# Kernel tuning notes

Hardware: AMD Instinct MI355X
Metric: run time of the kernel (lower is better)

The kernel has to match this reference:

```python
import jax, jax.numpy as jnp
import numpy as np

B = 8
A = 1614
TOPN = 6
IOU_THR = 0.25
PAD = 224
OUT = 224

def _make_anchors():
    # 6 anchor shapes on the 14x14 map, 6 on 7x7, 9 on 4x4 -> 1614 total,
    # ordered anchor-type-major then row-major spatial to match the [C,H,W] flatten
    # of the tidy conv outputs (as generate_default_anchor_maps does in NTS-Net).
    specs = [
        (14, 32.0, [(48, 48), (64, 48), (48, 64), (80, 80), (96, 64), (64, 96)]),
        (7, 64.0, [(96, 96), (128, 96), (96, 128), (160, 160), (192, 128), (128, 192)]),
        (4, 112.0, [(192, 192), (256, 192), (192, 256), (288, 288), (320, 256), (256, 320), (352, 352), (384, 320), (320, 384)]),
    ]
    blocks = []
    for fm, stride, sizes in specs:
        c = (np.arange(fm) + 0.5) * stride
        cy, cx = np.meshgrid(c, c, indexing='ij')
        for (h, w) in sizes:
            blocks.append(np.stack([cy - h / 2, cx - w / 2, cy + h / 2, cx + w / 2], -1).reshape(-1, 4))
    a = (np.concatenate(blocks, 0) + PAD).astype(np.int64)  # mimic (edge_anchors+224).astype(int)
    return a.astype(np.float32)  # [1614,4] (y0,x0,y1,x1) in padded-image coords

def _conv(x, w, b, stride, pad):
    y = jax.lax.conv_general_dilated(x, w, (stride, stride), [(pad, pad), (pad, pad)],
                                     dimension_numbers=('NCHW', 'OIHW', 'NCHW'))
    return y + b[None, :, None, None]

def _rpn_scores(rpn, wd1, bd1, wd2, bd2, wd3, bd3, wt1, bt1, wt2, bt2, wt3, bt3):
    b = rpn.shape[0]
    d1 = jax.nn.relu(_conv(rpn, wd1, bd1, 1, 1))   # [B,128,14,14]
    d2 = jax.nn.relu(_conv(d1, wd2, bd2, 2, 1))    # [B,128,7,7]
    d3 = jax.nn.relu(_conv(d2, wd3, bd3, 2, 1))    # [B,128,4,4]
    t1 = _conv(d1, wt1, bt1, 1, 0).reshape(b, -1)  # [B,1176]
    t2 = _conv(d2, wt2, bt2, 1, 0).reshape(b, -1)  # [B,294]
    t3 = _conv(d3, wt3, bt3, 1, 0).reshape(b, -1)  # [B,144]
    return jnp.concatenate([t1, t2, t3], axis=1)   # [B,1614]

def _nms_keep(boxes, scores):
    # Greedy NMS over all A anchors; returns keep mask in ORIGINAL anchor order.
    order = jnp.argsort(-scores)
    b = boxes[order]
    y0, x0, y1, x1 = b[:, 0], b[:, 1], b[:, 2], b[:, 3]
    area = (y1 - y0) * (x1 - x0)
    ih = jnp.clip(jnp.minimum(y1[:, None], y1[None, :]) - jnp.maximum(y0[:, None], y0[None, :]), 0)
    iw = jnp.clip(jnp.minimum(x1[:, None], x1[None, :]) - jnp.maximum(x0[:, None], x0[None, :]), 0)
    inter = ih * iw
    iou = inter / (area[:, None] + area[None, :] - inter)
    idx = jnp.arange(A)
    def body(i, supp):
        row = (iou[i] > IOU_THR) & (idx > i)
        return jnp.where(supp[i], supp, supp | row)
    supp = jax.lax.fori_loop(0, A, body, jnp.zeros((A,), bool))
    return jnp.zeros((A,), bool).at[order].set(~supp)

def _crop_resize(img, box):
    # img [3,Hp,Wp]; box int32 (x0,y0,x1,y1).
    # Equivalent to F.interpolate(img[:, y0:y1, x0:x1], (224,224), 'bilinear', align_corners=True)
    x0, y0, x1, y1 = box[0], box[1], box[2], box[3]
    t = jnp.arange(OUT, dtype=jnp.float32) / (OUT - 1)
    sy = y0.astype(jnp.float32) + t * (y1 - 1 - y0).astype(jnp.float32)
    sx = x0.astype(jnp.float32) + t * (x1 - 1 - x0).astype(jnp.float32)
    y0i = jnp.floor(sy).astype(jnp.int32); x0i = jnp.floor(sx).astype(jnp.int32)
    y1i = jnp.minimum(y0i + 1, y1 - 1);    x1i = jnp.minimum(x0i + 1, x1 - 1)
    wy = (sy - y0i.astype(jnp.float32))[None, :, None]
    wx = (sx - x0i.astype(jnp.float32))[None, None, :]
    g = lambda yi, xi: img[:, yi][:, :, xi]  # gather rows then cols -> [3,224,224]
    top = (1 - wx) * g(y0i, x0i) + wx * g(y0i, x1i)
    bot = (1 - wx) * g(y1i, x0i) + wx * g(y1i, x1i)
    return (1 - wy) * top + wy * bot

def setup_inputs():
    key = jax.random.key(0)
    ks = jax.random.split(key, 16)
    n = jax.random.normal
    return {
        'x': n(ks[0], (B, 3, 448, 448), jnp.float32),
        'rpn_feature': n(ks[1], (B, 2048, 14, 14), jnp.float32),
        'anchors': jnp.asarray(_make_anchors()),
        'wd1': 0.02 * n(ks[2], (128, 2048, 3, 3), jnp.float32), 'bd1': 0.01 * n(ks[3], (128,), jnp.float32),
        'wd2': 0.05 * n(ks[4], (128, 128, 3, 3), jnp.float32),  'bd2': 0.01 * n(ks[5], (128,), jnp.float32),
        'wd3': 0.05 * n(ks[6], (128, 128, 3, 3), jnp.float32),  'bd3': 0.01 * n(ks[7], (128,), jnp.float32),
        'wt1': 0.1 * n(ks[8], (6, 128, 1, 1), jnp.float32),     'bt1': 0.01 * n(ks[9], (6,), jnp.float32),
        'wt2': 0.1 * n(ks[10], (6, 128, 1, 1), jnp.float32),    'bt2': 0.01 * n(ks[11], (6,), jnp.float32),
        'wt3': 0.1 * n(ks[12], (9, 128, 1, 1), jnp.float32),    'bt3': 0.01 * n(ks[13], (9,), jnp.float32),
    }

def reference(x, rpn_feature, anchors, wd1, bd1, wd2, bd2, wd3, bd3, wt1, bt1, wt2, bt2, wt3, bt3):
    scores = _rpn_scores(rpn_feature, wd1, bd1, wd2, bd2, wd3, bd3, wt1, bt1, wt2, bt2, wt3, bt3)
    keep = jax.vmap(lambda s: _nms_keep(anchors, s))(scores)           # [B,A] bool
    masked = jnp.where(keep, scores, -jnp.inf)
    top_prob, top_idx = jax.lax.top_k(masked, TOPN)                    # [B,6]
    tb = anchors[top_idx]                                              # [B,6,4] (y0,x0,y1,x1)
    coords = jnp.stack([tb[..., 1], tb[..., 0], tb[..., 3], tb[..., 2]], -1)  # (x0,y0,x1,y1)
    x_pad = jnp.pad(x, ((0, 0), (0, 0), (PAD, PAD), (PAD, PAD)))       # [B,3,896,896]
    bint = coords.astype(jnp.int32)
    part_imgs = jax.vmap(lambda img, bs: jax.vmap(lambda bb: _crop_resize(img, bb))(bs))(x_pad, bint)  # [B,6,3,224,224]
    return part_imgs, coords, top_prob, top_idx
```

## Files before the change

### kernel.cpp

```cpp
#include <hip/hip_runtime.h>
#include <hip/hip_bf16.h>
#include <math.h>
#include <stdint.h>


#define OFF_COORDS 7225344
#define OFF_PROB   7225536
#define OFF_IDX    7225584
#define NA 1614
#define K1TOT 18432

typedef __attribute__((ext_vector_type(8)))  short  short8;
typedef __attribute__((ext_vector_type(16))) float  floatx16;

__global__ __launch_bounds__(256) void k_prep_a(const float* __restrict__ rpn,
                                                __hip_bfloat16* __restrict__ ah,
                                                __hip_bfloat16* __restrict__ al)
{
    __shared__ float tile[64][65];
    const int cib  = blockIdx.x * 64;
    const int posb = blockIdx.y * 64;
    const int b    = blockIdx.z;
    const int t    = threadIdx.x;
#pragma unroll
    for (int it = 0; it < 16; ++it) {
        int idx  = it * 256 + t;
        int cil  = idx >> 6;
        int posl = idx & 63;
        int pos  = posb + posl;
        int py = pos >> 4, px = pos & 15;
        int y = py - 1, x = px - 1;
        float v = 0.0f;
        if ((unsigned)y < 14u && (unsigned)x < 14u)
            v = rpn[((size_t)(b * 2048 + cib + cil) * 14 + y) * 14 + x];
        tile[cil][posl] = v;
    }
    __syncthreads();
#pragma unroll
    for (int it = 0; it < 16; ++it) {
        int idx  = it * 256 + t;
        int posl = idx >> 6;
        int cil  = idx & 63;
        float v = tile[cil][posl];
        __hip_bfloat16 h = __float2bfloat16(v);
        __hip_bfloat16 l = __float2bfloat16(v - __bfloat162float(h));
        size_t o = (size_t)(b * 256 + posb + posl) * 2048 + cib + cil;
        ah[o] = h; al[o] = l;
    }
}

__global__ __launch_bounds__(256) void k_prep_b(const float* __restrict__ w,
                                                __hip_bfloat16* __restrict__ bh,
                                                __hip_bfloat16* __restrict__ bl)
{
    const int tap = blockIdx.x;
    const int co  = blockIdx.y;
    const int t   = threadIdx.x;
#pragma unroll
    for (int i = 0; i < 8; ++i) {
        int ci = i * 256 + t;
        float v = w[((size_t)co * 2048 + ci) * 9 + tap];
        __hip_bfloat16 h = __float2bfloat16(v);
        __hip_bfloat16 l = __float2bfloat16(v - __bfloat162float(h));
        size_t o = (size_t)co * K1TOT + tap * 2048 + ci;
        bh[o] = h; bl[o] = l;
    }
}

__global__ __launch_bounds__(128) void k_prep_w23(const float* __restrict__ w2,
                                                  const float* __restrict__ w3,
                                                  __hip_bfloat16* __restrict__ b2h,
                                                  __hip_bfloat16* __restrict__ b2l,
                                                  __hip_bfloat16* __restrict__ b3h,
                                                  __hip_bfloat16* __restrict__ b3l)
{
    const int tap = blockIdx.x;
    const int co  = blockIdx.y;
    const int z   = blockIdx.z;
    const int ci  = threadIdx.x;
    const float* w = z ? w3 : w2;
    __hip_bfloat16* bh = z ? b3h : b2h;
    __hip_bfloat16* bl = z ? b3l : b2l;
    float v = w[((size_t)co * 128 + ci) * 9 + tap];
    __hip_bfloat16 h = __float2bfloat16(v);
    __hip_bfloat16 l = __float2bfloat16(v - __bfloat162float(h));
    size_t o = (size_t)co * 1152 + tap * 128 + ci;
    bh[o] = h; bl[o] = l;
}

template<int POSN, int OW, int STR, int CIN, int MTOT>
__global__ __launch_bounds__(256) void k_conv_mfma(const short* __restrict__ ah,
                                                   const short* __restrict__ al,
                                                   const short* __restrict__ bh,
                                                   const short* __restrict__ bl,
                                                   float* __restrict__ partial,
                                                   int chunk)
{
    constexpr int KTOT = CIN * 9;
    __shared__ short AsH[128][40];
    __shared__ short AsL[128][40];
    __shared__ short BsH[128][40];
    __shared__ short BsL[128][40];

    const int t     = threadIdx.x;
    const int lane  = t & 63;
    const int w     = t >> 6;
    const int wm    = (w & 1) * 64;
    const int wn    = (w >> 1) * 64;
    const int lm    = lane & 31;
    const int half  = lane >> 5;
    const int mbase = blockIdx.x * 128;
    const int k0    = blockIdx.y * chunk;
    const int k1    = (k0 + chunk < KTOT) ? (k0 + chunk) : KTOT;

    int arow[2], apos[2]; bool aval[2];
    const int akc = (t & 3) * 8;
#pragma unroll
    for (int i = 0; i < 2; ++i) {
        int row = ((i * 256 + t) >> 2);
        int m   = mbase + row;
        arow[i] = row;
        aval[i] = (m < MTOT);
        int mm = aval[i] ? m : 0;
        int b  = mm / POSN;
        int p  = mm - b * POSN;
        int y  = p / OW;
        int x  = p - y * OW;
        apos[i] = b * 256 + y * STR * 16 + x * STR;
    }

    floatx16 acc[2][2];
#pragma unroll
    for (int mf = 0; mf < 2; ++mf)
#pragma unroll
        for (int nf = 0; nf < 2; ++nf)
#pragma unroll
            for (int r = 0; r < 16; ++r) acc[mf][nf][r] = 0.0f;

    const short8 zero8 = {0, 0, 0, 0, 0, 0, 0, 0};

    for (int ks = k0; ks < k1; ks += 32) {
        const int tap = ks / CIN;
        const int ci0 = ks - tap * CIN;
        const int dy  = tap / 3, dx = tap - dy * 3;
#pragma unroll
        for (int i = 0; i < 2; ++i) {
            short8 vh = zero8, vl = zero8;
            if (aval[i]) {
                size_t g = (size_t)(apos[i] + dy * 16 + dx) * CIN + ci0 + akc;
                vh = *(const short8*)(ah + g);
                vl = *(const short8*)(al + g);
            }
            *(short8*)&AsH[arow[i]][akc] = vh;
            *(short8*)&AsL[arow[i]][akc] = vl;
        }
#pragma unroll
        for (int i = 0; i < 2; ++i) {
            int n = ((i * 256 + t) >> 2);
            size_t g = (size_t)n * KTOT + ks + akc;
            *(short8*)&BsH[n][akc] = *(const short8*)(bh + g);
            *(short8*)&BsL[n][akc] = *(const short8*)(bl + g);
        }
        __syncthreads();
#pragma unroll
        for (int kst = 0; kst < 2; ++kst) {
            const int koff = kst * 16 + half * 8;
            short8 a_h[2], a_l[2], b_h[2], b_l[2];
#pragma unroll
            for (int mf = 0; mf < 2; ++mf) {
                a_h[mf] = *(const short8*)&AsH[wm + mf * 32 + lm][koff];
                a_l[mf] = *(const short8*)&AsL[wm + mf * 32 + lm][koff];
            }
#pragma unroll
            for (int nf = 0; nf < 2; ++nf) {
                b_h[nf] = *(const short8*)&BsH[wn + nf * 32 + lm][koff];
                b_l[nf] = *(const short8*)&BsL[wn + nf * 32 + lm][koff];
            }
#pragma unroll
            for (int mf = 0; mf < 2; ++mf)
#pragma unroll
                for (int nf = 0; nf < 2; ++nf) {
                    acc[mf][nf] = __builtin_amdgcn_mfma_f32_32x32x16_bf16(
                        a_h[mf], b_h[nf], acc[mf][nf], 0, 0, 0);
                    acc[mf][nf] = __builtin_amdgcn_mfma_f32_32x32x16_bf16(
                        a_h[mf], b_l[nf], acc[mf][nf], 0, 0, 0);
                    acc[mf][nf] = __builtin_amdgcn_mfma_f32_32x32x16_bf16(
                        a_l[mf], b_h[nf], acc[mf][nf], 0, 0, 0);
                }
        }
        __syncthreads();
    }

    float* P = partial + (size_t)blockIdx.y * MTOT * 128;
#pragma unroll
    for (int mf = 0; mf < 2; ++mf)
#pragma unroll
        for (int nf = 0; nf < 2; ++nf)
#pragma unroll
            for (int r = 0; r < 16; ++r) {
                int row = (r & 3) + 8 * (r >> 2) + 4 * half;
                int m = mbase + wm + mf * 32 + row;
                int n = wn + nf * 32 + lm;
                if (m < MTOT) P[(size_t)m * 128 + n] = acc[mf][nf][r];
            }
}

template<int POSN, int OWV>
__global__ __launch_bounds__(256) void k_reduce_pad(const float* __restrict__ partial,
                                                    const float* __restrict__ bias,
                                                    float* __restrict__ dn,
                                                    __hip_bfloat16* __restrict__ ph,
                                                    __hip_bfloat16* __restrict__ pl,
                                                    int S)
{
    constexpr int MTOT = 8 * POSN;
    int idx = blockIdx.x * 256 + threadIdx.x;
    int b   = idx >> 15;
    int pos = (idx >> 7) & 255;
    int co  = idx & 127;
    int y = (pos >> 4) - 1;
    int x = (pos & 15) - 1;
    if ((unsigned)y < (unsigned)OWV && (unsigned)x < (unsigned)OWV) {
        int m = b * POSN + y * OWV + x;
        float s = bias[co];
        for (int k = 0; k < S; ++k) s += partial[(size_t)k * MTOT * 128 + m * 128 + co];
        s = fmaxf(s, 0.0f);
        dn[(size_t)m * 128 + co] = s;
        __hip_bfloat16 h = __float2bfloat16(s);
        __hip_bfloat16 l = __float2bfloat16(s - __bfloat162float(h));
        ph[idx] = h; pl[idx] = l;
    } else {
        ph[idx] = __float2bfloat16(0.0f);
        pl[idx] = __float2bfloat16(0.0f);
    }
}

__global__ __launch_bounds__(256) void k_reduce3(const float* __restrict__ partial,
                                                 const float* __restrict__ bias,
                                                 float* __restrict__ dn, int S)
{
    int idx = blockIdx.x * 256 + threadIdx.x;
    int co  = idx & 127;
    float s = bias[co];
    for (int k = 0; k < S; ++k) s += partial[(size_t)k * 128 * 128 + idx];
    dn[idx] = fmaxf(s, 0.0f);
}

__global__ __launch_bounds__(256) void k_heads(const float* __restrict__ d1n,
                                               const float* __restrict__ d2n,
                                               const float* __restrict__ d3n,
                                               const float* __restrict__ w1, const float* __restrict__ b1,
                                               const float* __restrict__ w2, const float* __restrict__ b2,
                                               const float* __restrict__ w3, const float* __restrict__ b3,
                                               float* __restrict__ scores)
{
    int idx = blockIdx.x * 256 + threadIdx.x;
    if (idx >= 8 * NA) return;
    int b = idx / NA;
    int e = idx - b * NA;
    const float* d; const float* w; float bias;
    if (e < 1176) {
        int c = e / 196, p = e - c * 196;
        d = d1n + (size_t)(b * 196 + p) * 128; w = w1 + c * 128; bias = b1[c];
    } else if (e < 1470) {
        int e2 = e - 1176; int c = e2 / 49, p = e2 - c * 49;
        d = d2n + (size_t)(b * 49 + p) * 128; w = w2 + c * 128; bias = b2[c];
    } else {
        int e2 = e - 1470; int c = e2 / 16, p = e2 - c * 16;
        d = d3n + (size_t)(b * 16 + p) * 128; w = w3 + c * 128; bias = b3[c];
    }
    float s = bias;
#pragma unroll
    for (int i = 0; i < 32; ++i) {
        float4 dv = ((const float4*)d)[i];
        float4 wv = ((const float4*)w)[i];
        s = fmaf(dv.x, wv.x, s);
        s = fmaf(dv.y, wv.y, s);
        s = fmaf(dv.z, wv.z, s);
        s = fmaf(dv.w, wv.w, s);
    }
    scores[idx] = s;
}

__global__ __launch_bounds__(256) void k_nms_topk(const float* __restrict__ scores,
                                                  const float* __restrict__ anchors,
                                                  float* __restrict__ out,
                                                  int* __restrict__ boxes)
{
    __shared__ float ms[NA];
    __shared__ float ay0[NA], ax0[NA], ay1[NA], ax1[NA];
    __shared__ unsigned char picked[NA];
    __shared__ float rv[4]; __shared__ int ri[4];
    __shared__ float win[5];
    int b = blockIdx.x;
    int t = threadIdx.x;
    for (int i = t; i < NA; i += 256) {
        ms[i] = scores[b * NA + i];
        float4 an = ((const float4*)anchors)[i];
        ay0[i] = an.x; ax0[i] = an.y; ay1[i] = an.z; ax1[i] = an.w;
        picked[i] = 0;
    }
    __syncthreads();
    for (int r = 0; r < 6; ++r) {
        float bv = -INFINITY; int bi = NA;
        for (int i = t; i < NA; i += 256) {
            if (!picked[i]) {
                float v = ms[i];
                if (v > bv || (v == bv && i < bi)) { bv = v; bi = i; }
            }
        }
#pragma unroll
        for (int off = 32; off > 0; off >>= 1) {
            float v2 = __shfl_down(bv, off);
            int   i2 = __shfl_down(bi, off);
            if (v2 > bv || (v2 == bv && i2 < bi)) { bv = v2; bi = i2; }
        }
        if ((t & 63) == 0) { rv[t >> 6] = bv; ri[t >> 6] = bi; }
        __syncthreads();
        if (t == 0) {
            bv = rv[0]; bi = ri[0];
            for (int wv = 1; wv < 4; ++wv)
                if (rv[wv] > bv || (rv[wv] == bv && ri[wv] < bi)) { bv = rv[wv]; bi = ri[wv]; }
            picked[bi] = 1;
            win[0] = ay0[bi]; win[1] = ax0[bi]; win[2] = ay1[bi]; win[3] = ax1[bi]; win[4] = bv;
            int o = b * 6 + r;
            out[OFF_COORDS + o * 4 + 0] = ax0[bi];
            out[OFF_COORDS + o * 4 + 1] = ay0[bi];
            out[OFF_COORDS + o * 4 + 2] = ax1[bi];
            out[OFF_COORDS + o * 4 + 3] = ay1[bi];
            out[OFF_PROB + o] = bv;
            out[OFF_IDX  + o] = (float)bi;
            boxes[o * 4 + 0] = (int)ax0[bi];
            boxes[o * 4 + 1] = (int)ay0[bi];
            boxes[o * 4 + 2] = (int)ax1[bi];
            boxes[o * 4 + 3] = (int)ay1[bi];
        }
        __syncthreads();
        float by0 = win[0], bx0 = win[1], by1 = win[2], bx1 = win[3];
        float barea = (by1 - by0) * (bx1 - bx0);
        for (int i = t; i < NA; i += 256) {
            if (picked[i]) continue;
            float ih = fmaxf(fminf(by1, ay1[i]) - fmaxf(by0, ay0[i]), 0.0f);
            float iw = fmaxf(fminf(bx1, ax1[i]) - fmaxf(bx0, ax0[i]), 0.0f);
            float inter = ih * iw;
            float area  = (ay1[i] - ay0[i]) * (ax1[i] - ax0[i]);
            float iou = inter / (barea + area - inter);
            if (iou > 0.25f) ms[i] = -INFINITY;
        }
        __syncthreads();
    }
}

__global__ __launch_bounds__(256) void k_crop(const float* __restrict__ x,
                                              const int* __restrict__ boxes,
                                              float* __restrict__ out)
{
    int bid = blockIdx.x;
    int i = threadIdx.x;
    if (i >= 224) return;
    int j   = bid % 224;
    int rem = bid / 224;
    int c   = rem % 3;
    int br  = rem / 3;
    int b   = br / 6;
    int4 bx = ((const int4*)boxes)[br];
    float tj = (float)j / 223.0f;
    float sy = (float)bx.y + tj * (float)(bx.w - 1 - bx.y);
    int y0i = (int)floorf(sy);
    int y1i = min(y0i + 1, bx.w - 1);
    float wy = sy - (float)y0i;
    float ti = (float)i / 223.0f;
    float sx = (float)bx.x + ti * (float)(bx.z - 1 - bx.x);
    int x0i = (int)floorf(sx);
    int x1i = min(x0i + 1, bx.z - 1);
    float wx = sx - (float)x0i;
    const float* img = x + ((size_t)b * 3 + c) * 448 * 448;
    auto g = [&](int yy, int xx) -> float {
        yy -= 224; xx -= 224;
        if ((unsigned)yy >= 448u || (unsigned)xx >= 448u) return 0.0f;
        return img[(size_t)yy * 448 + xx];
    };
    float g00 = g(y0i, x0i), g01 = g(y0i, x1i);
    float g10 = g(y1i, x0i), g11 = g(y1i, x1i);
    float top = (1.0f - wx) * g00 + wx * g01;
    float bot = (1.0f - wx) * g10 + wx * g11;
    out[(size_t)bid * 224 + i] = (1.0f - wy) * top + wy * bot;
}

extern "C" void kernel_launch(void* const* d_in, const int* in_sizes, int n_in,
                              void* d_out, int out_size, void* d_ws, size_t ws_size,
                              hipStream_t stream)
{
    (void)in_sizes; (void)n_in; (void)out_size;
    const float* x    = (const float*)d_in[0];
    const float* rpn  = (const float*)d_in[1];
    const float* anch = (const float*)d_in[2];
    const float* wd1  = (const float*)d_in[3];
    const float* bd1  = (const float*)d_in[4];
    const float* wd2  = (const float*)d_in[5];
    const float* bd2  = (const float*)d_in[6];
    const float* wd3  = (const float*)d_in[7];
    const float* bd3  = (const float*)d_in[8];
    const float* hw1  = (const float*)d_in[9];
    const float* hb1  = (const float*)d_in[10];
    const float* hw2  = (const float*)d_in[11];
    const float* hb2  = (const float*)d_in[12];
    const float* hw3  = (const float*)d_in[13];
    const float* hb3  = (const float*)d_in[14];
    float* out = (float*)d_out;

    char* ws = (char*)d_ws;
    size_t off = 0;
    auto alloc = [&](size_t bytes) -> void* {
        void* p = ws + off;
        off = (off + bytes + 255) & ~(size_t)255;
        return p;
    };
    __hip_bfloat16* ahb  = (__hip_bfloat16*)alloc((size_t)8 * 256 * 2048 * 2);
    __hip_bfloat16* alb  = (__hip_bfloat16*)alloc((size_t)8 * 256 * 2048 * 2);
    __hip_bfloat16* b1h  = (__hip_bfloat16*)alloc((size_t)128 * K1TOT * 2);
    __hip_bfloat16* b1l  = (__hip_bfloat16*)alloc((size_t)128 * K1TOT * 2);
    __hip_bfloat16* b2h  = (__hip_bfloat16*)alloc((size_t)128 * 1152 * 2);
    __hip_bfloat16* b2l  = (__hip_bfloat16*)alloc((size_t)128 * 1152 * 2);
    __hip_bfloat16* b3h  = (__hip_bfloat16*)alloc((size_t)128 * 1152 * 2);
    __hip_bfloat16* b3l  = (__hip_bfloat16*)alloc((size_t)128 * 1152 * 2);
    __hip_bfloat16* d1ph = (__hip_bfloat16*)alloc((size_t)8 * 256 * 128 * 2);
    __hip_bfloat16* d1pl = (__hip_bfloat16*)alloc((size_t)8 * 256 * 128 * 2);
    __hip_bfloat16* d2ph = (__hip_bfloat16*)alloc((size_t)8 * 256 * 128 * 2);
    __hip_bfloat16* d2pl = (__hip_bfloat16*)alloc((size_t)8 * 256 * 128 * 2);
    float* d1n  = (float*)alloc((size_t)8 * 196 * 128 * 4);
    float* d2n  = (float*)alloc((size_t)8 * 49 * 128 * 4);
    float* d3n  = (float*)alloc((size_t)8 * 16 * 128 * 4);
    float* sc   = (float*)alloc((size_t)8 * NA * 4);
    int*  boxes = (int*)alloc((size_t)8 * 6 * 4 * 4);
    size_t avail = (ws_size > off) ? (ws_size - off) : 0;
    float* P = (float*)(ws + off);

    long long s1 = (long long)(avail / ((size_t)1568 * 128 * 4));
    if (s1 > 48) s1 = 48;
    if (s1 < 1)  s1 = 1;
    int S1 = (int)s1;
    int chunk1 = ((K1TOT + S1 * 32 - 1) / (S1 * 32)) * 32;

    k_prep_b<<<dim3(9, 128), 256, 0, stream>>>(wd1, b1h, b1l);
    k_prep_w23<<<dim3(9, 128, 2), 128, 0, stream>>>(wd2, wd3, b2h, b2l, b3h, b3l);
    k_prep_a<<<dim3(32, 4, 8), 256, 0, stream>>>(rpn, ahb, alb);

    k_conv_mfma<196, 14, 1, 2048, 1568><<<dim3(13, S1), 256, 0, stream>>>(
        (const short*)ahb, (const short*)alb, (const short*)b1h, (const short*)b1l, P, chunk1);
    k_reduce_pad<196, 14><<<dim3(1024), 256, 0, stream>>>(P, bd1, d1n, d1ph, d1pl, S1);

    k_conv_mfma<49, 7, 2, 128, 392><<<dim3(4, 9), 256, 0, stream>>>(
        (const short*)d1ph, (const short*)d1pl, (const short*)b2h, (const short*)b2l, P, 128);
    k_reduce_pad<49, 7><<<dim3(1024), 256, 0, stream>>>(P, bd2, d2n, d2ph, d2pl, 9);

    k_conv_mfma<16, 4, 2, 128, 128><<<dim3(1, 9), 256, 0, stream>>>(
        (const short*)d2ph, (const short*)d2pl, (const short*)b3h, (const short*)b3l, P, 128);
    k_reduce3<<<dim3(64), 256, 0, stream>>>(P, bd3, d3n, 9);

    k_heads<<<dim3((8 * NA + 255) / 256), 256, 0, stream>>>(d1n, d2n, d3n,
        hw1, hb1, hw2, hb2, hw3, hb3, sc);
    k_nms_topk<<<dim3(8), 256, 0, stream>>>(sc, anch, out, boxes);
    k_crop<<<dim3(8 * 6 * 3 * 224), 256, 0, stream>>>(x, boxes, out);
}
```

Measured before the change: 259.1 us.

## Merge prep kernels, swizzle conv1 blocks per XCD, raise split-K, densify crop grid

Merges the three weight and activation prep kernels into one launch, which removes two launch boundaries. Conv1 now uses a 1D grid swizzled so that the k-chunks for one XCD stay together, which should help L2 reuse of the B slices. The split-K factor goes up to 64 when workspace allows. The crop kernel now maps threads linearly, so it no longer idles 32 of 256 threads per block. The trade-off is more partial-sum reduction traffic from the larger S1, and chunk1 now assumes K1TOT divides evenly by S1.

```diff
diff --git a/kernel.cpp b/kernel.cpp
--- a/kernel.cpp
+++ b/kernel.cpp
@@ -13,94 +13,105 @@
 typedef __attribute__((ext_vector_type(8)))  short  short8;
 typedef __attribute__((ext_vector_type(16))) float  floatx16;
 
-__global__ __launch_bounds__(256) void k_prep_a(const float* __restrict__ rpn,
-                                                __hip_bfloat16* __restrict__ ah,
-                                                __hip_bfloat16* __restrict__ al)
-{
-    __shared__ float tile[64][65];
-    const int cib  = blockIdx.x * 64;
-    const int posb = blockIdx.y * 64;
-    const int b    = blockIdx.z;
-    const int t    = threadIdx.x;
-#pragma unroll
-    for (int it = 0; it < 16; ++it) {
-        int idx  = it * 256 + t;
-        int cil  = idx >> 6;
-        int posl = idx & 63;
-        int pos  = posb + posl;
-        int py = pos >> 4, px = pos & 15;
-        int y = py - 1, x = px - 1;
-        float v = 0.0f;
-        if ((unsigned)y < 14u && (unsigned)x < 14u)
-            v = rpn[((size_t)(b * 2048 + cib + cil) * 14 + y) * 14 + x];
-        tile[cil][posl] = v;
-    }
-    __syncthreads();
-#pragma unroll
-    for (int it = 0; it < 16; ++it) {
-        int idx  = it * 256 + t;
-        int posl = idx >> 6;
-        int cil  = idx & 63;
-        float v = tile[cil][posl];
+__global__ __launch_bounds__(256) void k_prep_all(
+    const float* __restrict__ rpn,
+    const float* __restrict__ wd1,
+    const float* __restrict__ wd2,
+    const float* __restrict__ wd3,
+    __hip_bfloat16* __restrict__ ah,  __hip_bfloat16* __restrict__ al,
+    __hip_bfloat16* __restrict__ b1h, __hip_bfloat16* __restrict__ b1l,
+    __hip_bfloat16* __restrict__ b2h, __hip_bfloat16* __restrict__ b2l,
+    __hip_bfloat16* __restrict__ b3h, __hip_bfloat16* __restrict__ b3l)
+{
+    const int bid = blockIdx.x;
+    const int t   = threadIdx.x;
+    if (bid < 1024) {
+        __shared__ float tile[64][65];
+        const int cib  = (bid & 31) * 64;
+        const int posb = ((bid >> 5) & 3) * 64;
+        const int b    = bid >> 7;
+#pragma unroll
+        for (int it = 0; it < 16; ++it) {
+            int idx  = it * 256 + t;
+            int cil  = idx >> 6;
+            int posl = idx & 63;
+            int pos  = posb + posl;
+            int py = pos >> 4, px = pos & 15;
+            int y = py - 1, x = px - 1;
+            float v = 0.0f;
+            if ((unsigned)y < 14u && (unsigned)x < 14u)
+                v = rpn[((size_t)(b * 2048 + cib + cil) * 14 + y) * 14 + x];
+            tile[cil][posl] = v;
+        }
+        __syncthreads();
+#pragma unroll
+        for (int it = 0; it < 16; ++it) {
+            int idx  = it * 256 + t;
+            int posl = idx >> 6;
+            int cil  = idx & 63;
+            float v = tile[cil][posl];
+            __hip_bfloat16 h = __float2bfloat16(v);
+            __hip_bfloat16 l = __float2bfloat16(v - __bfloat162float(h));
+            size_t o = (size_t)(b * 256 + posb + posl) * 2048 + cib + cil;
+            ah[o] = h; al[o] = l;
+        }
+    } else if (bid < 2176) {
+        int local = bid - 1024;
+        int tap = local % 9;
+        int co  = local / 9;
+#pragma unroll
+        for (int i = 0; i < 8; ++i) {
+            int ci = i * 256 + t;
+            float v = wd1[((size_t)co * 2048 + ci) * 9 + tap];
+            __hip_bfloat16 h = __float2bfloat16(v);
+            __hip_bfloat16 l = __float2bfloat16(v - __bfloat162float(h));
+            size_t o = (size_t)co * K1TOT + tap * 2048 + ci;
+            b1h[o] = h; b1l[o] = l;
+        }
+    } else {
+        int local = bid - 2176;
+        int z  = local >= 576;
+        int l3 = z ? (local - 576) : local;
+        int tap = l3 % 9;
+        int co  = (l3 / 9) * 2 + (t >> 7);
+        int ci  = t & 127;
+        const float* w = z ? wd3 : wd2;
+        __hip_bfloat16* bh = z ? b3h : b2h;
+        __hip_bfloat16* bl = z ? b3l : b2l;
+        float v = w[((size_t)co * 128 + ci) * 9 + tap];
         __hip_bfloat16 h = __float2bfloat16(v);
         __hip_bfloat16 l = __float2bfloat16(v - __bfloat162float(h));
-        size_t o = (size_t)(b * 256 + posb + posl) * 2048 + cib + cil;
-        ah[o] = h; al[o] = l;
-    }
-}
-
-__global__ __launch_bounds__(256) void k_prep_b(const float* __restrict__ w,
-                                                __hip_bfloat16* __restrict__ bh,
-                                                __hip_bfloat16* __restrict__ bl)
-{
-    const int tap = blockIdx.x;
-    const int co  = blockIdx.y;
-    const int t   = threadIdx.x;
-#pragma unroll
-    for (int i = 0; i < 8; ++i) {
-        int ci = i * 256 + t;
-        float v = w[((size_t)co * 2048 + ci) * 9 + tap];
-        __hip_bfloat16 h = __float2bfloat16(v);
-        __hip_bfloat16 l = __float2bfloat16(v - __bfloat162float(h));
-        size_t o = (size_t)co * K1TOT + tap * 2048 + ci;
+        size_t o = (size_t)co * 1152 + tap * 128 + ci;
         bh[o] = h; bl[o] = l;
     }
 }
 
-__global__ __launch_bounds__(128) void k_prep_w23(const float* __restrict__ w2,
-                                                  const float* __restrict__ w3,
-                                                  __hip_bfloat16* __restrict__ b2h,
-                                                  __hip_bfloat16* __restrict__ b2l,
-                                                  __hip_bfloat16* __restrict__ b3h,
-                                                  __hip_bfloat16* __restrict__ b3l)
-{
-    const int tap = blockIdx.x;
-    const int co  = blockIdx.y;
-    const int z   = blockIdx.z;
-    const int ci  = threadIdx.x;
-    const float* w = z ? w3 : w2;
-    __hip_bfloat16* bh = z ? b3h : b2h;
-    __hip_bfloat16* bl = z ? b3l : b2l;
-    float v = w[((size_t)co * 128 + ci) * 9 + tap];
-    __hip_bfloat16 h = __float2bfloat16(v);
-    __hip_bfloat16 l = __float2bfloat16(v - __bfloat162float(h));
-    size_t o = (size_t)co * 1152 + tap * 128 + ci;
-    bh[o] = h; bl[o] = l;
-}
-
-template<int POSN, int OW, int STR, int CIN, int MTOT>
+template<int POSN, int OW, int STR, int CIN, int MTOT, bool SWIZ>
 __global__ __launch_bounds__(256) void k_conv_mfma(const short* __restrict__ ah,
                                                    const short* __restrict__ al,
                                                    const short* __restrict__ bh,
                                                    const short* __restrict__ bl,
                                                    float* __restrict__ partial,
-                                                   int chunk)
+                                                   int chunk, int kpx, int mtiles)
 {
     constexpr int KTOT = CIN * 9;
     __shared__ short AsH[128][40];
     __shared__ short AsL[128][40];
     __shared__ short BsH[128][40];
     __shared__ short BsL[128][40];
+
+    int mt, kc;
+    if (SWIZ) {
+        int bid = blockIdx.x;
+        int xcd = bid & 7;
+        int idx = bid >> 3;
+        int q   = idx / mtiles;
+        kc = xcd * kpx + q;
+        mt = idx - q * mtiles;
+    } else {
+        mt = blockIdx.x;
+        kc = blockIdx.y;
+    }
 
     const int t     = threadIdx.x;
     const int lane  = t & 63;
@@ -109,8 +120,8 @@
     const int wn    = (w >> 1) * 64;
     const int lm    = lane & 31;
     const int half  = lane >> 5;
-    const int mbase = blockIdx.x * 128;
-    const int k0    = blockIdx.y * chunk;
+    const int mbase = mt * 128;
+    const int k0    = kc * chunk;
     const int k1    = (k0 + chunk < KTOT) ? (k0 + chunk) : KTOT;
 
     int arow[2], apos[2]; bool aval[2];
@@ -191,7 +202,7 @@
         __syncthreads();
     }
 
-    float* P = partial + (size_t)blockIdx.y * MTOT * 128;
+    float* P = partial + (size_t)kc * MTOT * 128;
 #pragma unroll
     for (int mf = 0; mf < 2; ++mf)
 #pragma unroll
@@ -355,14 +366,14 @@
                                               const int* __restrict__ boxes,
                                               float* __restrict__ out)
 {
-    int bid = blockIdx.x;
-    int i = threadIdx.x;
-    if (i >= 224) return;
-    int j   = bid % 224;
-    int rem = bid / 224;
-    int c   = rem % 3;
-    int br  = rem / 3;
-    int b   = br / 6;
+    int lin = blockIdx.x * 256 + threadIdx.x;
+    int i    = lin % 224;
+    int rest = lin / 224;
+    int j    = rest % 224;
+    int rc   = rest / 224;
+    int c    = rc % 3;
+    int br   = rc / 3;
+    int b    = br / 6;
     int4 bx = ((const int4*)boxes)[br];
     float tj = (float)j / 223.0f;
     float sy = (float)bx.y + tj * (float)(bx.w - 1 - bx.y);
@@ -384,7 +395,7 @@
     float g10 = g(y1i, x0i), g11 = g(y1i, x1i);
     float top = (1.0f - wx) * g00 + wx * g01;
     float bot = (1.0f - wx) * g10 + wx * g11;
-    out[(size_t)bid * 224 + i] = (1.0f - wy) * top + wy * bot;
+    out[lin] = (1.0f - wy) * top + wy * bot;
 }
 
 extern "C" void kernel_launch(void* const* d_in, const int* in_sizes, int n_in,
@@ -436,30 +447,31 @@
     size_t avail = (ws_size > off) ? (ws_size - off) : 0;
     float* P = (float*)(ws + off);
 
-    long long s1 = (long long)(avail / ((size_t)1568 * 128 * 4));
-    if (s1 > 48) s1 = 48;
-    if (s1 < 1)  s1 = 1;
-    int S1 = (int)s1;
-    int chunk1 = ((K1TOT + S1 * 32 - 1) / (S1 * 32)) * 32;
-
-    k_prep_b<<<dim3(9, 128), 256, 0, stream>>>(wd1, b1h, b1l);
-    k_prep_w23<<<dim3(9, 128, 2), 128, 0, stream>>>(wd2, wd3, b2h, b2l, b3h, b3l);
-    k_prep_a<<<dim3(32, 4, 8), 256, 0, stream>>>(rpn, ahb, alb);
-
-    k_conv_mfma<196, 14, 1, 2048, 1568><<<dim3(13, S1), 256, 0, stream>>>(
-        (const short*)ahb, (const short*)alb, (const short*)b1h, (const short*)b1l, P, chunk1);
+    int S1 = (avail >= (size_t)64 * 1568 * 128 * 4) ? 64 : 48;
+    if (avail < (size_t)48 * 1568 * 128 * 4) S1 = 32;
+    int chunk1 = K1TOT / S1;
+    int kpx1   = S1 / 8;
+
+    k_prep_all<<<dim3(3328), 256, 0, stream>>>(rpn, wd1, wd2, wd3,
+        ahb, alb, b1h, b1l, b2h, b2l, b3h, b3l);
+
+    k_conv_mfma<196, 14, 1, 2048, 1568, true><<<dim3(13 * S1), 256, 0, stream>>>(
+        (const short*)ahb, (const short*)alb, (const short*)b1h, (const short*)b1l,
+        P, chunk1, kpx1, 13);
     k_reduce_pad<196, 14><<<dim3(1024), 256, 0, stream>>>(P, bd1, d1n, d1ph, d1pl, S1);
 
-    k_conv_mfma<49, 7, 2, 128, 392><<<dim3(4, 9), 256, 0, stream>>>(
-        (const short*)d1ph, (const short*)d1pl, (const short*)b2h, (const short*)b2l, P, 128);
+    k_conv_mfma<49, 7, 2, 128, 392, false><<<dim3(4, 9), 256, 0, stream>>>(
+        (const short*)d1ph, (const short*)d1pl, (const short*)b2h, (const short*)b2l,
+        P, 128, 0, 0);
     k_reduce_pad<49, 7><<<dim3(1024), 256, 0, stream>>>(P, bd2, d2n, d2ph, d2pl, 9);
 
-    k_conv_mfma<16, 4, 2, 128, 128><<<dim3(1, 9), 256, 0, stream>>>(
-        (const short*)d2ph, (const short*)d2pl, (const short*)b3h, (const short*)b3l, P, 128);
+    k_conv_mfma<16, 4, 2, 128, 128, false><<<dim3(1, 9), 256, 0, stream>>>(
+        (const short*)d2ph, (const short*)d2pl, (const short*)b3h, (const short*)b3l,
+        P, 128, 0, 0);
     k_reduce3<<<dim3(64), 256, 0, stream>>>(P, bd3, d3n, 9);
 
     k_heads<<<dim3((8 * NA + 255) / 256), 256, 0, stream>>>(d1n, d2n, d3n,
         hw1, hb1, hw2, hb2, hw3, hb3, sc);
     k_nms_topk<<<dim3(8), 256, 0, stream>>>(sc, anch, out, boxes);
-    k_crop<<<dim3(8 * 6 * 3 * 224), 256, 0, stream>>>(x, boxes, out);
-}
+    k_crop<<<dim3(28224), 256, 0, stream>>>(x, boxes, out);
+}
```

Measured after the change: 268.6 us. 3.7% more time.
